# Kernel optimization log

Hardware: AMD Instinct MI355X
Metric: run time of the kernel (lower is better)

The kernel has to match this reference:

```python
import jax, jax.numpy as jnp
import numpy as np

N = 50000
E = 800000
EPS = 1e-16
NEG_SLOPE = 0.2

def setup_inputs() -> dict:
    key = jax.random.key(0)
    ks = jax.random.split(key, 10)
    s = lambda fan: 1.0 / np.sqrt(fan)
    return {
        "x": jax.random.normal(ks[0], (N, 128), dtype=jnp.float32),
        "edge_index": jax.random.randint(ks[1], (2, E), 0, N, dtype=jnp.int64),
        "W1": jax.random.normal(ks[2], (128, 4 * 32), dtype=jnp.float32) * s(128),
        "att_src1": jax.random.normal(ks[3], (4, 32), dtype=jnp.float32) * s(32),
        "att_dst1": jax.random.normal(ks[4], (4, 32), dtype=jnp.float32) * s(32),
        "b1": jnp.zeros((128,), dtype=jnp.float32),
        "W2": jax.random.normal(ks[5], (128, 2), dtype=jnp.float32) * s(128),
        "att_src2": jax.random.normal(ks[6], (1, 2), dtype=jnp.float32) * s(2),
        "att_dst2": jax.random.normal(ks[7], (1, 2), dtype=jnp.float32) * s(2),
        "b2": jnp.zeros((2,), dtype=jnp.float32),
    }

def _gat_conv(x, src, dst, W, att_src, att_dst, bias, heads, out_ch, concat):
    n = x.shape[0]
    h = (x @ W).reshape(n, heads, out_ch)                      # [N,H,C]
    a_src = jnp.sum(h * att_src[None], axis=-1)                # [N,H]
    a_dst = jnp.sum(h * att_dst[None], axis=-1)                # [N,H]
    e = jax.nn.leaky_relu(a_src[src] + a_dst[dst], NEG_SLOPE)  # [Etot,H]
    # segment softmax over incoming edges per destination node
    m = jax.ops.segment_max(e, dst, num_segments=n)            # [N,H]
    m = jnp.where(jnp.isfinite(m), m, 0.0)
    ex = jnp.exp(e - m[dst])
    denom = jax.ops.segment_sum(ex, dst, num_segments=n)       # [N,H]
    alpha = ex / (denom[dst] + EPS)                            # [Etot,H]
    out = jax.ops.segment_sum(alpha[:, :, None] * h[src], dst, num_segments=n)  # [N,H,C]
    if concat:
        out = out.reshape(n, heads * out_ch)
    else:
        out = out.mean(axis=1)
    return out + bias

def reference(x, edge_index, W1, att_src1, att_dst1, b1, W2, att_src2, att_dst2, b2):
    n = x.shape[0]
    # PyG GATConv adds self-loops by default
    loops = jnp.arange(n, dtype=edge_index.dtype)
    src = jnp.concatenate([edge_index[0], loops])
    dst = jnp.concatenate([edge_index[1], loops])
    # dropout is identity at inference
    h = jax.nn.elu(_gat_conv(x, src, dst, W1, att_src1, att_dst1, b1, 4, 32, True))
    h = _gat_conv(h, src, dst, W2, att_src2, att_dst2, b2, 1, 2, False)
    return jax.nn.log_softmax(h, axis=1)
```

## Files before the change

### kernel.cpp

```cpp
#include <hip/hip_runtime.h>
#include <hip/hip_bf16.h>

#define NN 50000
#define EE 800000
#define CAP 64
#define CSTRIDE 16
#define NEG_SLOPE 0.2f
#define EPSF 1e-16f
#define BUILD_BLOCKS 4096
#define GEMM_BLOCKS ((NN + 63) / 64)
#define NPAIRS (EE / 2)
#define WROW 136

typedef unsigned int uint32;
typedef __attribute__((ext_vector_type(8))) short short8;
typedef __attribute__((ext_vector_type(4))) float floatx4;

__device__ __forceinline__ unsigned short f2bf(float f) {
  unsigned int u = __float_as_uint(f);
  unsigned int r = (u + 0x7fffu + ((u >> 16) & 1u)) >> 16;
  return (unsigned short)r;
}
__device__ __forceinline__ float bf_lo(uint32 v) { return __uint_as_float(v << 16); }
__device__ __forceinline__ float bf_hi(uint32 v) { return __uint_as_float(v & 0xffff0000u); }
__device__ __forceinline__ float lrelu(float e) { return fmaxf(e, NEG_SLOPE * e); }

__device__ __forceinline__ void do_build(int b, const int* __restrict__ ei,
                                         int* __restrict__ counts,
                                         int* __restrict__ csr) {
  const int range = b & 7;
  const int lo = range * (NN / 8);
  const int hi = lo + (NN / 8);
  const int group = b >> 3;
  const int tid0 = group * 256 + threadIdx.x;
  const int stride = (BUILD_BLOCKS >> 3) * 256;

  { int n = lo + tid0; if (n < hi) csr[n * CAP] = n; }

  const int2* __restrict__ dst2 = (const int2*)(ei + EE);
  const int2* __restrict__ src2 = (const int2*)(ei);
  for (int p = tid0; p < NPAIRS; p += stride) {
    int2 d2 = dst2[p];
    int2 s2 = src2[p];
    if (d2.x >= lo && d2.x < hi) {
      int r = atomicAdd(&counts[d2.x * CSTRIDE], 1);
      if (r < CAP - 1) csr[d2.x * CAP + r + 1] = s2.x;
    }
    if (d2.y >= lo && d2.y < hi) {
      int r = atomicAdd(&counts[d2.y * CSTRIDE], 1);
      if (r < CAP - 1) csr[d2.y * CAP + r + 1] = s2.y;
    }
  }
}

__device__ __forceinline__ void do_gemm_tile(
    int tile, const float* __restrict__ x, const unsigned short* __restrict__ WtL,
    const float* __restrict__ att_src1, const float* __restrict__ att_dst1,
    uint32* __restrict__ h1b, float* __restrict__ as1, float* __restrict__ ad1) {
  const int t    = threadIdx.x;
  const int wave = t >> 6;
  const int lane = t & 63;
  const int quad = lane >> 4;
  const int col  = lane & 15;
  const int nodeBase = tile * 64 + wave * 16;

  floatx4 acc[8];
  #pragma unroll
  for (int i = 0; i < 8; i++) acc[i] = (floatx4){0.f, 0.f, 0.f, 0.f};

  int mread = nodeBase + col; if (mread >= NN) mread = NN - 1;
  const float* __restrict__ xrow = x + (size_t)mread * 128 + quad * 8;
  const unsigned short* __restrict__ bbase = WtL + col * WROW + quad * 8;

  #pragma unroll
  for (int ks = 0; ks < 4; ks++) {
    float4 a0 = *(const float4*)(xrow + ks * 32);
    float4 a1 = *(const float4*)(xrow + ks * 32 + 4);
    union { short8 v; unsigned short u[8]; } af;
    af.u[0] = f2bf(a0.x); af.u[1] = f2bf(a0.y);
    af.u[2] = f2bf(a0.z); af.u[3] = f2bf(a0.w);
    af.u[4] = f2bf(a1.x); af.u[5] = f2bf(a1.y);
    af.u[6] = f2bf(a1.z); af.u[7] = f2bf(a1.w);
    #pragma unroll
    for (int tt = 0; tt < 8; tt++) {
      short8 bf = *(const short8*)(bbase + tt * 16 * WROW + ks * 32);
      acc[tt] = __builtin_amdgcn_mfma_f32_16x16x32_bf16(af.v, bf, acc[tt], 0, 0, 0);
    }
  }

  float asv[8], adv[8];
  #pragma unroll
  for (int tt = 0; tt < 8; tt++) {
    asv[tt] = att_src1[tt * 16 + col];
    adv[tt] = att_dst1[tt * 16 + col];
  }

  #pragma unroll
  for (int r = 0; r < 4; r++) {
    const int gn = nodeBase + quad * 4 + r;
    const bool live = (gn < NN);
    #pragma unroll
    for (int tt = 0; tt < 8; tt++) {
      float v = acc[tt][r];
      float w = __shfl_xor(v, 1, 64);
      if (live && ((col & 1) == 0)) {
        uint32 pk = (uint32)f2bf(v) | ((uint32)f2bf(w) << 16);
        h1b[(size_t)gn * 64 + tt * 8 + (col >> 1)] = pk;
      }
    }
    #pragma unroll
    for (int h = 0; h < 4; h++) {
      float ps = acc[2 * h][r] * asv[2 * h] + acc[2 * h + 1][r] * asv[2 * h + 1];
      float pd = acc[2 * h][r] * adv[2 * h] + acc[2 * h + 1][r] * adv[2 * h + 1];
      #pragma unroll
      for (int off = 1; off < 16; off <<= 1) {
        ps += __shfl_xor(ps, off, 64);
        pd += __shfl_xor(pd, off, 64);
      }
      if (live && col == 0) {
        as1[gn * 4 + h] = ps;
        ad1[gn * 4 + h] = pd;
      }
    }
  }
}

__global__ __launch_bounds__(256) void work_k(
    const int* __restrict__ ei, int* __restrict__ counts, int* __restrict__ csr,
    const float* __restrict__ x, const float* __restrict__ W1,
    const float* __restrict__ att_src1, const float* __restrict__ att_dst1,
    uint32* __restrict__ h1b, float* __restrict__ as1, float* __restrict__ ad1) {
  __shared__ unsigned short WtL[128 * WROW];
  const int b = blockIdx.x;
  if (b < GEMM_BLOCKS) {
    const int c  = threadIdx.x & 127;
    const int kh = (threadIdx.x >> 7) * 4;
    #pragma unroll
    for (int k0 = kh; k0 < 128; k0 += 8) {
      unsigned short w0 = f2bf(W1[(k0 + 0) * 128 + c]);
      unsigned short w1 = f2bf(W1[(k0 + 1) * 128 + c]);
      unsigned short w2 = f2bf(W1[(k0 + 2) * 128 + c]);
      unsigned short w3 = f2bf(W1[(k0 + 3) * 128 + c]);
      uint32 lo = (uint32)w0 | ((uint32)w1 << 16);
      uint32 hi = (uint32)w2 | ((uint32)w3 << 16);
      *(uint2*)&WtL[c * WROW + k0] = make_uint2(lo, hi);
    }
    __syncthreads();
    do_gemm_tile(b, x, WtL, att_src1, att_dst1, h1b, as1, ad1);
  } else {
    do_build(b - GEMM_BLOCKS, ei, counts, csr);
  }
}

__global__ __launch_bounds__(256) void agg1_k(
    const int* __restrict__ counts, const int* __restrict__ csr,
    const uint32* __restrict__ h1b, const float* __restrict__ as1,
    const float* __restrict__ ad1, const float* __restrict__ b1,
    const float* __restrict__ W2, const float* __restrict__ att_src2,
    const float* __restrict__ att_dst2, float4* __restrict__ rec) {
  const int lane = threadIdx.x & 63;
  const int wv = threadIdx.x >> 6;
  const int hd = lane >> 4;
  const int n = __builtin_amdgcn_readfirstlane(blockIdx.x * 4 + wv);

  int cnt = counts[n * CSTRIDE] + 1;
  cnt = __builtin_amdgcn_readfirstlane(cnt < CAP ? cnt : CAP);
  const int* __restrict__ row = csr + n * CAP;
  const float adv = ad1[n * 4 + hd];

  float den = 0.f, accx = 0.f, accy = 0.f;
  int j = 0;
  for (; j + 3 < cnt; j += 4) {
    int s0 = __builtin_amdgcn_readfirstlane(row[j]);
    int s1 = __builtin_amdgcn_readfirstlane(row[j + 1]);
    int s2 = __builtin_amdgcn_readfirstlane(row[j + 2]);
    int s3 = __builtin_amdgcn_readfirstlane(row[j + 3]);
    float e0 = as1[s0 * 4 + hd] + adv;
    float e1 = as1[s1 * 4 + hd] + adv;
    float e2 = as1[s2 * 4 + hd] + adv;
    float e3 = as1[s3 * 4 + hd] + adv;
    uint32 v0 = h1b[s0 * 64 + lane];
    uint32 v1 = h1b[s1 * 64 + lane];
    uint32 v2 = h1b[s2 * 64 + lane];
    uint32 v3 = h1b[s3 * 64 + lane];
    e0 = lrelu(e0); e1 = lrelu(e1); e2 = lrelu(e2); e3 = lrelu(e3);
    float x0 = __expf(e0), x1 = __expf(e1), x2 = __expf(e2), x3 = __expf(e3);
    den += (x0 + x1) + (x2 + x3);
    accx = fmaf(x0, bf_lo(v0), accx);
    accy = fmaf(x0, bf_hi(v0), accy);
    accx = fmaf(x1, bf_lo(v1), accx);
    accy = fmaf(x1, bf_hi(v1), accy);
    accx = fmaf(x2, bf_lo(v2), accx);
    accy = fmaf(x2, bf_hi(v2), accy);
    accx = fmaf(x3, bf_lo(v3), accx);
    accy = fmaf(x3, bf_hi(v3), accy);
  }
  for (; j < cnt; j++) {
    int s = __builtin_amdgcn_readfirstlane(row[j]);
    float e = lrelu(as1[s * 4 + hd] + adv);
    float ex = __expf(e);
    uint32 v = h1b[s * 64 + lane];
    den += ex;
    accx = fmaf(ex, bf_lo(v), accx);
    accy = fmaf(ex, bf_hi(v), accy);
  }

  float inv = 1.f / (den + EPSF);
  float2 bb = ((const float2*)b1)[lane];
  float ox = accx * inv + bb.x;
  float oy = accy * inv + bb.y;
  ox = (ox > 0.f) ? ox : (__expf(ox) - 1.f);
  oy = (oy > 0.f) ? oy : (__expf(oy) - 1.f);

  float4 wq = ((const float4*)W2)[lane];
  float p0 = ox * wq.x + oy * wq.z;
  float p1 = ox * wq.y + oy * wq.w;
  #pragma unroll
  for (int off = 32; off; off >>= 1) {
    p0 += __shfl_xor(p0, off, 64);
    p1 += __shfl_xor(p1, off, 64);
  }
  if (lane == 0) {
    rec[n] = make_float4(p0, p1,
                         p0 * att_src2[0] + p1 * att_src2[1],
                         p0 * att_dst2[0] + p1 * att_dst2[1]);
  }
}

__global__ __launch_bounds__(256) void agg2_k(
    const int* __restrict__ counts, const int* __restrict__ csr,
    const float4* __restrict__ rec, const float* __restrict__ b2,
    float* __restrict__ out) {
  int i = blockIdx.x * 256 + threadIdx.x;
  if (i >= NN * 8) return;
  int n = i >> 3;
  int sub = i & 7;
  const float adv = rec[n].w;
  int cnt = counts[n * CSTRIDE] + 1;
  cnt = cnt < CAP ? cnt : CAP;
  const int* __restrict__ row = csr + n * CAP;

  float den = 0.f, a0 = 0.f, a1 = 0.f;
  for (int j = sub; j < cnt; j += 8) {
    int s = row[j];
    float4 rs = rec[s];
    float e = lrelu(rs.z + adv);
    float ex = __expf(e);
    den += ex;
    a0 = fmaf(ex, rs.x, a0);
    a1 = fmaf(ex, rs.y, a1);
  }
  #pragma unroll
  for (int off = 4; off; off >>= 1) {
    den += __shfl_down(den, off, 8);
    a0  += __shfl_down(a0, off, 8);
    a1  += __shfl_down(a1, off, 8);
  }
  if (sub == 0) {
    float inv = 1.f / (den + EPSF);
    float o0 = a0 * inv + b2[0];
    float o1 = a1 * inv + b2[1];
    float mx = fmaxf(o0, o1);
    float lse = mx + __logf(__expf(o0 - mx) + __expf(o1 - mx));
    *(float2*)&out[n * 2] = make_float2(o0 - lse, o1 - lse);
  }
}

extern "C" void kernel_launch(void* const* d_in, const int* in_sizes, int n_in,
                              void* d_out, int out_size, void* d_ws, size_t ws_size,
                              hipStream_t stream) {
  const float* x        = (const float*)d_in[0];
  const int*   ei       = (const int*)d_in[1];
  const float* W1       = (const float*)d_in[2];
  const float* att_src1 = (const float*)d_in[3];
  const float* att_dst1 = (const float*)d_in[4];
  const float* b1       = (const float*)d_in[5];
  const float* W2       = (const float*)d_in[6];
  const float* att_src2 = (const float*)d_in[7];
  const float* att_dst2 = (const float*)d_in[8];
  const float* b2       = (const float*)d_in[9];
  float* out = (float*)d_out;

  char* p = (char*)d_ws;
  auto alloc = [&](size_t bytes) {
    char* r = p;
    p += (bytes + 255) & ~size_t(255);
    return r;
  };
  uint32* h1b  = (uint32*)alloc(sizeof(uint32) * NN * 64);
  float* as1   = (float*)alloc(sizeof(float) * NN * 4);
  float* ad1   = (float*)alloc(sizeof(float) * NN * 4);
  float4* rec  = (float4*)alloc(sizeof(float4) * NN);
  int*   counts = (int*)alloc(sizeof(int) * NN * CSTRIDE);
  int*   csr   = (int*)alloc(sizeof(int) * NN * CAP);

  hipMemsetAsync(counts, 0, sizeof(int) * NN * CSTRIDE, stream);
  work_k<<<GEMM_BLOCKS + BUILD_BLOCKS, 256, 0, stream>>>(
      ei, counts, csr, x, W1, att_src1, att_dst1, h1b, as1, ad1);
  agg1_k<<<NN / 4, 256, 0, stream>>>(counts, csr, h1b, as1, ad1, b1, W2,
                                     att_src2, att_dst2, rec);
  agg2_k<<<(NN * 8 + 255) / 256, 256, 0, stream>>>(counts, csr, rec, b2, out);
}
```

Before: 172.1 us.

## Split wavefront into two half-waves processing alternate edges with 8-byte gathers

The layer-1 aggregation kernel now splits each 64-lane wavefront into two halves. Each half handles alternate neighbor edges, and each lane gathers a uint2 holding four bf16 features. The two halves' partial sums are combined with a cross-half shuffle, and the final W2 projection reduction uses offsets within 32 lanes. The CSR build also drops from 8 to 4 destination ranges, so each block rescans the edge list fewer times, at the cost of more atomic contention per range. The aim is more memory-level parallelism per wave and fewer serial loop iterations per node.

```diff
diff --git a/kernel.cpp b/kernel.cpp
--- a/kernel.cpp
+++ b/kernel.cpp
@@ -11,6 +11,7 @@
 #define GEMM_BLOCKS ((NN + 63) / 64)
 #define NPAIRS (EE / 2)
 #define WROW 136
+#define NRANGE 4
 
 typedef unsigned int uint32;
 typedef __attribute__((ext_vector_type(8))) short short8;
@@ -28,12 +29,12 @@
 __device__ __forceinline__ void do_build(int b, const int* __restrict__ ei,
                                          int* __restrict__ counts,
                                          int* __restrict__ csr) {
-  const int range = b & 7;
-  const int lo = range * (NN / 8);
-  const int hi = lo + (NN / 8);
-  const int group = b >> 3;
+  const int range = b & (NRANGE - 1);
+  const int lo = range * (NN / NRANGE);
+  const int hi = lo + (NN / NRANGE);
+  const int group = b >> 2;
   const int tid0 = group * 256 + threadIdx.x;
-  const int stride = (BUILD_BLOCKS >> 3) * 256;
+  const int stride = (BUILD_BLOCKS / NRANGE) * 256;
 
   { int n = lo + tid0; if (n < hi) csr[n * CAP] = n; }
 
@@ -159,64 +160,75 @@
     const float* __restrict__ W2, const float* __restrict__ att_src2,
     const float* __restrict__ att_dst2, float4* __restrict__ rec) {
   const int lane = threadIdx.x & 63;
-  const int wv = threadIdx.x >> 6;
-  const int hd = lane >> 4;
+  const int wv   = threadIdx.x >> 6;
+  const int half = lane >> 5;
+  const int l2   = lane & 31;
+  const int hd   = l2 >> 3;
   const int n = __builtin_amdgcn_readfirstlane(blockIdx.x * 4 + wv);
 
   int cnt = counts[n * CSTRIDE] + 1;
   cnt = __builtin_amdgcn_readfirstlane(cnt < CAP ? cnt : CAP);
   const int* __restrict__ row = csr + n * CAP;
   const float adv = ad1[n * 4 + hd];
-
-  float den = 0.f, accx = 0.f, accy = 0.f;
-  int j = 0;
-  for (; j + 3 < cnt; j += 4) {
-    int s0 = __builtin_amdgcn_readfirstlane(row[j]);
-    int s1 = __builtin_amdgcn_readfirstlane(row[j + 1]);
-    int s2 = __builtin_amdgcn_readfirstlane(row[j + 2]);
-    int s3 = __builtin_amdgcn_readfirstlane(row[j + 3]);
-    float e0 = as1[s0 * 4 + hd] + adv;
-    float e1 = as1[s1 * 4 + hd] + adv;
-    float e2 = as1[s2 * 4 + hd] + adv;
-    float e3 = as1[s3 * 4 + hd] + adv;
-    uint32 v0 = h1b[s0 * 64 + lane];
-    uint32 v1 = h1b[s1 * 64 + lane];
-    uint32 v2 = h1b[s2 * 64 + lane];
-    uint32 v3 = h1b[s3 * 64 + lane];
-    e0 = lrelu(e0); e1 = lrelu(e1); e2 = lrelu(e2); e3 = lrelu(e3);
-    float x0 = __expf(e0), x1 = __expf(e1), x2 = __expf(e2), x3 = __expf(e3);
-    den += (x0 + x1) + (x2 + x3);
-    accx = fmaf(x0, bf_lo(v0), accx);
-    accy = fmaf(x0, bf_hi(v0), accy);
-    accx = fmaf(x1, bf_lo(v1), accx);
-    accy = fmaf(x1, bf_hi(v1), accy);
-    accx = fmaf(x2, bf_lo(v2), accx);
-    accy = fmaf(x2, bf_hi(v2), accy);
-    accx = fmaf(x3, bf_lo(v3), accx);
-    accy = fmaf(x3, bf_hi(v3), accy);
-  }
-  for (; j < cnt; j++) {
-    int s = __builtin_amdgcn_readfirstlane(row[j]);
+  const uint2* __restrict__ h1v = (const uint2*)h1b;
+
+  float den = 0.f;
+  float a0 = 0.f, a1 = 0.f, a2 = 0.f, a3 = 0.f;
+  int j0 = 0;
+  for (; j0 + 3 < cnt; j0 += 4) {
+    int sA = row[j0 + half];
+    int sB = row[j0 + 2 + half];
+    float eA = lrelu(as1[sA * 4 + hd] + adv);
+    float eB = lrelu(as1[sB * 4 + hd] + adv);
+    uint2 vA = h1v[sA * 32 + l2];
+    uint2 vB = h1v[sB * 32 + l2];
+    float xA = __expf(eA), xB = __expf(eB);
+    den += xA + xB;
+    a0 = fmaf(xA, bf_lo(vA.x), a0);
+    a1 = fmaf(xA, bf_hi(vA.x), a1);
+    a2 = fmaf(xA, bf_lo(vA.y), a2);
+    a3 = fmaf(xA, bf_hi(vA.y), a3);
+    a0 = fmaf(xB, bf_lo(vB.x), a0);
+    a1 = fmaf(xB, bf_hi(vB.x), a1);
+    a2 = fmaf(xB, bf_lo(vB.y), a2);
+    a3 = fmaf(xB, bf_hi(vB.y), a3);
+  }
+  for (int j = j0 + half; j < cnt; j += 2) {
+    int s = row[j];
     float e = lrelu(as1[s * 4 + hd] + adv);
     float ex = __expf(e);
-    uint32 v = h1b[s * 64 + lane];
+    uint2 v = h1v[s * 32 + l2];
     den += ex;
-    accx = fmaf(ex, bf_lo(v), accx);
-    accy = fmaf(ex, bf_hi(v), accy);
-  }
+    a0 = fmaf(ex, bf_lo(v.x), a0);
+    a1 = fmaf(ex, bf_hi(v.x), a1);
+    a2 = fmaf(ex, bf_lo(v.y), a2);
+    a3 = fmaf(ex, bf_hi(v.y), a3);
+  }
+
+  den += __shfl_xor(den, 32, 64);
+  a0  += __shfl_xor(a0, 32, 64);
+  a1  += __shfl_xor(a1, 32, 64);
+  a2  += __shfl_xor(a2, 32, 64);
+  a3  += __shfl_xor(a3, 32, 64);
 
   float inv = 1.f / (den + EPSF);
-  float2 bb = ((const float2*)b1)[lane];
-  float ox = accx * inv + bb.x;
-  float oy = accy * inv + bb.y;
-  ox = (ox > 0.f) ? ox : (__expf(ox) - 1.f);
-  oy = (oy > 0.f) ? oy : (__expf(oy) - 1.f);
-
-  float4 wq = ((const float4*)W2)[lane];
-  float p0 = ox * wq.x + oy * wq.z;
-  float p1 = ox * wq.y + oy * wq.w;
-  #pragma unroll
-  for (int off = 32; off; off >>= 1) {
+  float4 bb = ((const float4*)b1)[l2];
+  float o0 = fmaf(a0, inv, bb.x);
+  float o1 = fmaf(a1, inv, bb.y);
+  float o2 = fmaf(a2, inv, bb.z);
+  float o3 = fmaf(a3, inv, bb.w);
+  o0 = (o0 > 0.f) ? o0 : (__expf(o0) - 1.f);
+  o1 = (o1 > 0.f) ? o1 : (__expf(o1) - 1.f);
+  o2 = (o2 > 0.f) ? o2 : (__expf(o2) - 1.f);
+  o3 = (o3 > 0.f) ? o3 : (__expf(o3) - 1.f);
+
+  const float4* __restrict__ W2v = (const float4*)W2;
+  float4 wA = W2v[2 * l2];
+  float4 wB = W2v[2 * l2 + 1];
+  float p0 = o0 * wA.x + o1 * wA.z + o2 * wB.x + o3 * wB.z;
+  float p1 = o0 * wA.y + o1 * wA.w + o2 * wB.y + o3 * wB.w;
+  #pragma unroll
+  for (int off = 1; off < 32; off <<= 1) {
     p0 += __shfl_xor(p0, off, 64);
     p1 += __shfl_xor(p1, off, 64);
   }
```

New measurement: 176.5 us. +2.6%, slower.
